# Optimization experiments

Hardware: AMD Instinct MI355X
Metric: run time of the kernel (lower is better)

The kernel has to match this reference:

```python
import jax, jax.numpy as jnp
import numpy as np

COND_EPS = 1e-12  # singularity threshold for the 2x2 Hessian determinant


def setup_inputs() -> dict:
    key = jax.random.key(0)
    k1, k2 = jax.random.split(key)
    b, h, w = 8, 1024, 1536
    # neur_beta_eme: non-negative-ish network output (forward clamps at 0 anyway)
    neur_beta_eme = jax.random.uniform(k1, (b, 1, h, w), dtype=jnp.float32) * 2.0
    base_detector_score = jax.random.normal(k2, (b, 1, h, w), dtype=jnp.float32)
    return {
        "neur_beta_eme": neur_beta_eme,
        "base_detector_score": base_detector_score,
        "n": 2048,
        "border_size": 16,
    }


def _gather(score_flat, y, x, w):
    # score_flat: [b, h*w]; y,x: [b,n] -> [b,n]
    return jnp.take_along_axis(score_flat, y * w + x, axis=-1)


def reference(neur_beta_eme, base_detector_score, n, border_size):
    b, _, h, w = base_detector_score.shape
    # NeSSDetector.forward: model(image)[-1].clamp(min=0)
    neur = jnp.maximum(neur_beta_eme, 0.0)
    score = base_detector_score

    # base_detector.get_extrema_mask: 3x3 NMS (local max) + border exclusion
    pooled = jax.lax.reduce_window(score, -jnp.inf, jax.lax.max,
                                   (1, 1, 3, 3), (1, 1, 1, 1), "SAME")
    ys = jnp.arange(h)
    xs = jnp.arange(w)
    border = (((ys >= border_size) & (ys < h - border_size))[:, None]
              & ((xs >= border_size) & (xs < w - border_size))[None, :])
    extrema_mask = (score == pooled) & border[None, None]

    # ness_extrema_map = exp(-neur_beta_eme) * extrema_mask
    ness = jnp.exp(-neur) * extrema_mask.astype(score.dtype)

    # topk over flattened spatial dims
    ness_flat = ness.reshape(b, -1)                      # [b, h*w]
    _, flat_cand_kp = jax.lax.top_k(ness_flat, n)        # [b, n]

    # flat2grid(flat, w) + 0.5  (pixel-center coords, (y, x) order)
    y = flat_cand_kp // w
    x = flat_cand_kp % w
    cand_kp = jnp.stack([y, x], axis=-1).astype(score.dtype) + 0.5  # [b, n, 2]

    # localize_keypoints_via_taylor: 3x3 finite-difference gradient/Hessian,
    # solve H @ inc = -g per keypoint (2x2 closed-form solve)
    sf = score.reshape(b, -1)
    yc = jnp.clip(y, 1, h - 2)
    xc = jnp.clip(x, 1, w - 2)
    s00 = _gather(sf, yc, xc, w)
    sp0 = _gather(sf, yc + 1, xc, w)
    sm0 = _gather(sf, yc - 1, xc, w)
    s0p = _gather(sf, yc, xc + 1, w)
    s0m = _gather(sf, yc, xc - 1, w)
    spp = _gather(sf, yc + 1, xc + 1, w)
    spm = _gather(sf, yc + 1, xc - 1, w)
    smp = _gather(sf, yc - 1, xc + 1, w)
    smm = _gather(sf, yc - 1, xc - 1, w)

    gy = 0.5 * (sp0 - sm0)
    gx = 0.5 * (s0p - s0m)
    hyy = sp0 - 2.0 * s00 + sm0
    hxx = s0p - 2.0 * s00 + s0m
    hxy = 0.25 * (spp - spm - smp + smm)

    det = hyy * hxx - hxy * hxy
    sing_mask = jnp.abs(det) > COND_EPS
    safe_det = jnp.where(sing_mask, det, 1.0)
    inc_y = -(hxx * gy - hxy * gx) / safe_det
    inc_x = -(hyy * gx - hxy * gy) / safe_det
    inc = jnp.stack([inc_y, inc_x], axis=-1)             # [b, n, 2]
    inc = jnp.clip(jnp.where(sing_mask[..., None], inc, 0.0), -0.5, 0.5)

    kp = cand_kp + inc                                   # [b, n, 2]

    # kp_neur_beta_eme = neur.view(b,-1).gather(-1, flat_cand_kp)
    kp_neur = jnp.take_along_axis(neur.reshape(b, -1), flat_cand_kp, axis=-1)

    return jnp.concatenate([kp, kp_neur[..., None]], axis=-1)  # [b, n, 3]
```

## Files before the change

### kernel.cpp

```cpp
#include <hip/hip_runtime.h>
#include <math.h>

typedef unsigned int u32;
typedef unsigned long long u64;

#define B 8
#define H 1024
#define W 1536
#define NPIX (H * W)
#define NK 2048
#define BORDER 16
#define NSEG 64
#define TY 8
#define NTILE 6
#define GRIDY 31
#define HBINS 512
#define TOPK_CAP 4096
#define SORT_N 4096
#define SORT_T 512
#define SEG_CAP_MAX 4096
#define CTR_PAD 32
#define IDX_MASK 0x1FFFFFu

#define OFF_TCOUNT 128
#define OFF_HIST   4096
#define OFF_SEGCNT 20480
#define OFF_KEYS   86016
#define OFF_SORTED 348160
#define OFF_CAND   479232

__global__ __launch_bounds__(256) void cand_k(const float* __restrict__ neur,
                                              const float* __restrict__ score,
                                              u32* __restrict__ candp,
                                              u32* __restrict__ segcnt,
                                              u32* __restrict__ hist, int seg_cap) {
    __shared__ u32 lh[HBINS];
    int tile = blockIdx.x;
    int b = blockIdx.z;
    int wave = threadIdx.x >> 6;
    int lane = threadIdx.x & 63;
    for (int i = threadIdx.x; i < HBINS; i += 256) lh[i] = 0;
    __syncthreads();

    int strip = blockIdx.y * 4 + wave;
    int y0 = BORDER + strip * TY;
    int x0 = tile * 256 + lane * 4;
    const float* s = score + (size_t)b * NPIX;
    const float* nb = neur + (size_t)b * NPIX;
    bool haveL = (tile > 0) && (lane == 0);
    bool haveR = (tile < NTILE - 1) && (lane == 63);

    float4 rv[TY + 2];
    float le[TY + 2], re[TY + 2];
    const float* base_row = s + (size_t)(y0 - 1) * W + x0;
    #pragma unroll
    for (int r = 0; r < TY + 2; ++r) rv[r] = *(const float4*)(base_row + (size_t)r * W);
    #pragma unroll
    for (int r = 0; r < TY + 2; ++r) {
        le[r] = haveL ? base_row[(size_t)r * W - 1] : 0.0f;
        re[r] = haveR ? base_row[(size_t)r * W + 4] : 0.0f;
    }

    bool xok[4];
    #pragma unroll
    for (int e = 0; e < 4; ++e) {
        int x = x0 + e;
        xok[e] = (x >= BORDER) && (x < W - BORDER);
    }

    u32 extbits = 0;
    {
        float4 hm, h0, hp;
        #pragma unroll
        for (int r = 0; r < 2; ++r) {
            float4 c = rv[r];
            float l = __shfl_up(c.w, 1); if (haveL) l = le[r];
            float rr = __shfl_down(c.x, 1); if (haveR) rr = re[r];
            float4 hh;
            hh.x = fmaxf(fmaxf(l, c.x), c.y);
            hh.y = fmaxf(fmaxf(c.x, c.y), c.z);
            hh.z = fmaxf(fmaxf(c.y, c.z), c.w);
            hh.w = fmaxf(fmaxf(c.z, c.w), rr);
            if (r == 0) hm = hh; else h0 = hh;
        }
        #pragma unroll
        for (int ys = 0; ys < TY; ++ys) {
            float4 c = rv[ys + 2];
            float l = __shfl_up(c.w, 1); if (haveL) l = le[ys + 2];
            float rr = __shfl_down(c.x, 1); if (haveR) rr = re[ys + 2];
            hp.x = fmaxf(fmaxf(l, c.x), c.y);
            hp.y = fmaxf(fmaxf(c.x, c.y), c.z);
            hp.z = fmaxf(fmaxf(c.y, c.z), c.w);
            hp.w = fmaxf(fmaxf(c.z, c.w), rr);
            float pv[4];
            pv[0] = fmaxf(fmaxf(hm.x, h0.x), hp.x);
            pv[1] = fmaxf(fmaxf(hm.y, h0.y), hp.y);
            pv[2] = fmaxf(fmaxf(hm.z, h0.z), hp.z);
            pv[3] = fmaxf(fmaxf(hm.w, h0.w), hp.w);
            float4 c0 = rv[ys + 1];
            float cv[4] = {c0.x, c0.y, c0.z, c0.w};
            #pragma unroll
            for (int e = 0; e < 4; ++e)
                if (xok[e] && cv[e] >= pv[e]) extbits |= (1u << (ys * 4 + e));
            hm = h0; h0 = hp;
        }
    }

    u32 c = (u32)__popc(extbits);
    u32 scan = c;
    #pragma unroll
    for (int off = 1; off < 64; off <<= 1) {
        u32 o = (u32)__shfl_up((int)scan, off, 64);
        if (lane >= off) scan += o;
    }
    u32 excl = scan - c;
    u32 tot = (u32)__shfl((int)scan, 63, 64);
    if (tot) {
        int seg = (strip * NTILE + tile) & (NSEG - 1);
        u32* ctr = &segcnt[(u32)(b * NSEG + seg) * CTR_PAD];
        u32 base = 0;
        if (lane == 63) base = atomicAdd(ctr, scan);
        base = (u32)__shfl((int)base, 63, 64);
        u32 pos0 = base + excl;
        u32 sbase = (u32)(b * NSEG + seg) * (u32)seg_cap;
        u32 idxbase = (u32)(y0 * W + x0);
        #pragma unroll
        for (int k = 0; k < 32; ++k) {
            if (extbits & (1u << k)) {
                u32 idx = idxbase + (u32)(k >> 2) * W + (u32)(k & 3);
                float nv = fmaxf(nb[idx], 0.0f);
                u32 fb = __float_as_uint(nv);
                u32 bin = fb >> 21; if (bin > HBINS - 1) bin = HBINS - 1;
                atomicAdd(&lh[bin], 1u);
                u32 p = pos0 + (u32)__popc(extbits & ((1u << k) - 1u));
                if ((int)p < seg_cap) candp[sbase + p] = (bin << 21) | idx;
            }
        }
    }
    __syncthreads();
    for (int i = threadIdx.x; i < HBINS; i += 256) {
        u32 v = lh[i];
        if (v) atomicAdd(&hist[(u32)b * HBINS + i], v);
    }
}

__global__ __launch_bounds__(256) void compact_k(const u32* __restrict__ candp,
                                                 const u32* __restrict__ segcnt,
                                                 const u32* __restrict__ hist,
                                                 const float* __restrict__ neur,
                                                 u64* __restrict__ keysout,
                                                 u32* tcount, int seg_cap) {
    __shared__ u32 piv_s;
    int seg = blockIdx.x;
    int b = blockIdx.y;
    int lane = threadIdx.x & 63;
    if (threadIdx.x < 64) {
        if (threadIdx.x == 0) piv_s = 0xFFFFFFFFu;
        u32 v[8];
        u32 s8 = 0;
        #pragma unroll
        for (int e = 0; e < 8; ++e) {
            v[e] = hist[(u32)b * HBINS + (u32)threadIdx.x * 8u + e];
            s8 += v[e];
        }
        u32 incl = s8;
        #pragma unroll
        for (int off = 1; off < 64; off <<= 1) {
            u32 o = (u32)__shfl_up((int)incl, off, 64);
            if (lane >= off) incl += o;
        }
        u32 excl = incl - s8;
        if (excl < NK && incl >= NK) {
            u32 cum = excl;
            u32 T = 0;
            #pragma unroll
            for (int e = 0; e < 8; ++e) {
                cum += v[e];
                if (cum >= NK) { T = (u32)threadIdx.x * 8u + e; break; }
            }
            piv_s = (T + 2u) << 21;
        }
    }
    __syncthreads();
    u32 piv = piv_s;
    const float* nb = neur + (size_t)b * NPIX;

    u32 cnt = segcnt[(u32)(b * NSEG + seg) * CTR_PAD];
    if ((int)cnt > seg_cap) cnt = (u32)seg_cap;
    u32 base = (u32)(b * NSEG + seg) * (u32)seg_cap;
    u32 iters = (cnt + 255u) / 256u;
    for (u32 it = 0; it < iters; ++it) {
        u32 i = it * 256u + threadIdx.x;
        bool f = false;
        u32 idx = 0;
        if (i < cnt) {
            u32 p = candp[base + i];
            f = (p < piv);
            idx = p & IDX_MASK;
        }
        u64 m = __ballot((int)f);
        if (m) {
            int leader = __ffsll((long long)m) - 1;
            u32 wbase = 0;
            if (lane == leader) wbase = atomicAdd(&tcount[b * CTR_PAD], (u32)__popcll(m));
            wbase = (u32)__shfl((int)wbase, leader, 64);
            if (f) {
                u32 pos = wbase + (u32)__popcll(m & ((1ull << (u32)lane) - 1ull));
                if (pos < TOPK_CAP) {
                    float nv = fmaxf(nb[idx], 0.0f);
                    float ness = (float)exp(-(double)nv);
                    keysout[(u32)b * TOPK_CAP + pos] =
                        ((u64)__float_as_uint(ness) << 32) | (u32)(~idx);
                }
            }
        }
    }
}

__device__ __forceinline__ u32 sw(u32 i) { return i + (i >> 4); }

__device__ __forceinline__ void cex(u64& a, u64& b, bool desc) {
    bool swp = desc ? (a < b) : (a > b);
    if (swp) { u64 tmp = a; a = b; b = tmp; }
}

__global__ __launch_bounds__(SORT_T) void sort_k(const u64* __restrict__ keysin,
                                                 const u32* __restrict__ tcount,
                                                 u64* __restrict__ sorted) {
    __shared__ u64 keys[SORT_N + (SORT_N >> 4)];
    int b = blockIdx.x;
    u32 t = threadIdx.x;
    u32 cnt = tcount[b * CTR_PAD];
    if (cnt > TOPK_CAP) cnt = TOPK_CAP;
    for (u32 i = t; i < SORT_N; i += SORT_T)
        keys[sw(i)] = (i < cnt) ? keysin[(u32)b * TOPK_CAP + i] : 0ull;
    __syncthreads();

    {
        u64 r[8];
        u32 base = t * 8u;
        #pragma unroll
        for (int e = 0; e < 8; ++e) r[e] = keys[sw(base + e)];
        cex(r[0], r[1], true);  cex(r[2], r[3], false);
        cex(r[4], r[5], true);  cex(r[6], r[7], false);
        cex(r[0], r[2], true);  cex(r[1], r[3], true);
        cex(r[4], r[6], false); cex(r[5], r[7], false);
        cex(r[0], r[1], true);  cex(r[2], r[3], true);
        cex(r[4], r[5], false); cex(r[6], r[7], false);
        bool d = ((base & 8u) == 0u);
        cex(r[0], r[4], d); cex(r[1], r[5], d); cex(r[2], r[6], d); cex(r[3], r[7], d);
        cex(r[0], r[2], d); cex(r[1], r[3], d); cex(r[4], r[6], d); cex(r[5], r[7], d);
        cex(r[0], r[1], d); cex(r[2], r[3], d); cex(r[4], r[5], d); cex(r[6], r[7], d);
        #pragma unroll
        for (int e = 0; e < 8; ++e) keys[sw(base + e)] = r[e];
    }
    __syncthreads();

    for (u32 k = 16; k <= SORT_N; k <<= 1) {
        u32 j = k >> 1;
        while (j >= 4) {
            u32 j0 = j >> 2;
            u32 base = ((t & ~(j0 - 1u)) << 3) | (t & (j0 - 1u));
            bool d = ((base & k) == 0u);
            u64 r[8];
            #pragma unroll
            for (int e = 0; e < 8; ++e) r[e] = keys[sw(base + (u32)e * j0)];
            cex(r[0], r[4], d); cex(r[1], r[5], d); cex(r[2], r[6], d); cex(r[3], r[7], d);
            cex(r[0], r[2], d); cex(r[1], r[3], d); cex(r[4], r[6], d); cex(r[5], r[7], d);
            cex(r[0], r[1], d); cex(r[2], r[3], d); cex(r[4], r[5], d); cex(r[6], r[7], d);
            #pragma unroll
            for (int e = 0; e < 8; ++e) keys[sw(base + (u32)e * j0)] = r[e];
            __syncthreads();
            j >>= 3;
        }
        if (j == 2) {
            #pragma unroll
            for (u32 m = 0; m < 2; ++m) {
                u32 vt = t + m * SORT_T;
                u32 base = vt << 2;
                bool d = ((base & k) == 0u);
                u64 r0 = keys[sw(base)], r1 = keys[sw(base + 1)];
                u64 r2 = keys[sw(base + 2)], r3 = keys[sw(base + 3)];
                cex(r0, r2, d); cex(r1, r3, d);
                cex(r0, r1, d); cex(r2, r3, d);
                keys[sw(base)] = r0; keys[sw(base + 1)] = r1;
                keys[sw(base + 2)] = r2; keys[sw(base + 3)] = r3;
            }
            __syncthreads();
        } else if (j == 1) {
            #pragma unroll
            for (u32 m = 0; m < 4; ++m) {
                u32 vt = t + m * SORT_T;
                u32 base = vt << 1;
                bool d = ((base & k) == 0u);
                u64 r0 = keys[sw(base)], r1 = keys[sw(base + 1)];
                cex(r0, r1, d);
                keys[sw(base)] = r0; keys[sw(base + 1)] = r1;
            }
            __syncthreads();
        }
    }

    for (u32 i = t; i < NK; i += SORT_T)
        sorted[(u32)b * NK + i] = keys[sw(i)];
}

__global__ __launch_bounds__(256) void refine_k(const float* __restrict__ neur,
                                                const float* __restrict__ score,
                                                const u64* __restrict__ sorted,
                                                float* __restrict__ out) {
    int b = blockIdx.y;
    u32 i = blockIdx.x * 256u + threadIdx.x;
    const float* s = score + (size_t)b * NPIX;
    const float* nb = neur + (size_t)b * NPIX;
    u64 key = sorted[(u32)b * NK + i];
    u32 idx = ~(u32)key;
    int y = (int)(idx / W), x = (int)(idx % W);
    int yc = min(max(y, 1), H - 2), xc = min(max(x, 1), W - 2);
    int p = yc * W + xc;
    float s00 = s[p], sp0 = s[p + W], sm0 = s[p - W], s0p = s[p + 1], s0m = s[p - 1];
    float spp = s[p + W + 1], spm = s[p + W - 1], smp = s[p - W + 1], smm = s[p - W - 1];
    float gy = 0.5f * (sp0 - sm0);
    float gx = 0.5f * (s0p - s0m);
    float hyy = sp0 - 2.0f * s00 + sm0;
    float hxx = s0p - 2.0f * s00 + s0m;
    float hxy = 0.25f * (spp - spm - smp + smm);
    float det = hyy * hxx - hxy * hxy;
    bool sing = fabsf(det) > 1e-12f;
    float sd = sing ? det : 1.0f;
    float iy = -(hxx * gy - hxy * gx) / sd;
    float ix = -(hyy * gx - hxy * gy) / sd;
    if (!sing) { iy = 0.0f; ix = 0.0f; }
    iy = fminf(fmaxf(iy, -0.5f), 0.5f);
    ix = fminf(fmaxf(ix, -0.5f), 0.5f);
    size_t o = ((size_t)b * NK + (size_t)i) * 3;
    out[o] = (float)y + 0.5f + iy;
    out[o + 1] = (float)x + 0.5f + ix;
    out[o + 2] = fmaxf(nb[idx], 0.0f);
}

extern "C" void kernel_launch(void* const* d_in, const int* in_sizes, int n_in,
                              void* d_out, int out_size, void* d_ws, size_t ws_size,
                              hipStream_t stream) {
    const float* neur = (const float*)d_in[0];
    const float* score = (const float*)d_in[1];
    float* out = (float*)d_out;
    char* ws = (char*)d_ws;
    u32* tcount = (u32*)(ws + OFF_TCOUNT);
    u32* hist = (u32*)(ws + OFF_HIST);
    u32* segcnt = (u32*)(ws + OFF_SEGCNT);
    u64* keysbuf = (u64*)(ws + OFF_KEYS);
    u64* sorted = (u64*)(ws + OFF_SORTED);
    u32* candp = (u32*)(ws + OFF_CAND);

    size_t avail = ws_size > OFF_CAND ? ws_size - OFF_CAND : 0;
    long long cap_ll = (long long)(avail / (4ull * B * NSEG));
    int seg_cap = cap_ll > SEG_CAP_MAX ? SEG_CAP_MAX : (int)cap_ll;

    hipMemsetAsync(ws, 0, OFF_KEYS, stream);
    cand_k<<<dim3(NTILE, GRIDY, B), 256, 0, stream>>>(neur, score, candp, segcnt, hist, seg_cap);
    compact_k<<<dim3(NSEG, B), 256, 0, stream>>>(candp, segcnt, hist, neur, keysbuf, tcount, seg_cap);
    sort_k<<<B, SORT_T, 0, stream>>>(keysbuf, tcount, sorted);
    refine_k<<<dim3(NK / 256, B), 256, 0, stream>>>(neur, score, sorted, out);
}
```

Before: 189.1 us.

## Replace per-batch bitonic sort with parallel rank-counting and scatter by rank

Removes the single-block-per-batch bitonic sort, whose many barrier-separated passes occupy only eight workgroups. In its place a rank kernel runs many 1024-thread blocks: each key counts how many keys in a tile are larger and accumulates that count atomically. Refine then writes each candidate whose rank is below the top-k count directly to its output slot. The candidate kernel also preloads neur rows as float4 vectors instead of doing scattered scalar loads. The cost is O(N^2) comparisons and a larger memset that now clears the key buffer so empty slots hold zero keys.

```diff
diff --git a/kernel.cpp b/kernel.cpp
--- a/kernel.cpp
+++ b/kernel.cpp
@@ -16,8 +16,6 @@
 #define GRIDY 31
 #define HBINS 512
 #define TOPK_CAP 4096
-#define SORT_N 4096
-#define SORT_T 512
 #define SEG_CAP_MAX 4096
 #define CTR_PAD 32
 #define IDX_MASK 0x1FFFFFu
@@ -25,8 +23,8 @@
 #define OFF_TCOUNT 128
 #define OFF_HIST   4096
 #define OFF_SEGCNT 20480
-#define OFF_KEYS   86016
-#define OFF_SORTED 348160
+#define OFF_RANK   86016
+#define OFF_KEYS   217088
 #define OFF_CAND   479232
 
 __global__ __launch_bounds__(256) void cand_k(const float* __restrict__ neur,
@@ -51,10 +49,14 @@
     bool haveR = (tile < NTILE - 1) && (lane == 63);
 
     float4 rv[TY + 2];
+    float4 nvv[TY];
     float le[TY + 2], re[TY + 2];
     const float* base_row = s + (size_t)(y0 - 1) * W + x0;
+    const float* nrow = nb + (size_t)y0 * W + x0;
     #pragma unroll
     for (int r = 0; r < TY + 2; ++r) rv[r] = *(const float4*)(base_row + (size_t)r * W);
+    #pragma unroll
+    for (int r = 0; r < TY; ++r) nvv[r] = *(const float4*)(nrow + (size_t)r * W);
     #pragma unroll
     for (int r = 0; r < TY + 2; ++r) {
         le[r] = haveL ? base_row[(size_t)r * W - 1] : 0.0f;
@@ -127,11 +129,14 @@
         #pragma unroll
         for (int k = 0; k < 32; ++k) {
             if (extbits & (1u << k)) {
-                u32 idx = idxbase + (u32)(k >> 2) * W + (u32)(k & 3);
-                float nv = fmaxf(nb[idx], 0.0f);
+                const int ro = k >> 2, e = k & 3;
+                float4 nq = nvv[ro];
+                float raw = (e == 0) ? nq.x : (e == 1) ? nq.y : (e == 2) ? nq.z : nq.w;
+                float nv = fmaxf(raw, 0.0f);
                 u32 fb = __float_as_uint(nv);
                 u32 bin = fb >> 21; if (bin > HBINS - 1) bin = HBINS - 1;
                 atomicAdd(&lh[bin], 1u);
+                u32 idx = idxbase + (u32)ro * W + (u32)e;
                 u32 p = pos0 + (u32)__popc(extbits & ((1u << k) - 1u));
                 if ((int)p < seg_cap) candp[sbase + p] = (bin << 21) | idx;
             }
@@ -217,104 +222,34 @@
     }
 }
 
-__device__ __forceinline__ u32 sw(u32 i) { return i + (i >> 4); }
-
-__device__ __forceinline__ void cex(u64& a, u64& b, bool desc) {
-    bool swp = desc ? (a < b) : (a > b);
-    if (swp) { u64 tmp = a; a = b; b = tmp; }
-}
-
-__global__ __launch_bounds__(SORT_T) void sort_k(const u64* __restrict__ keysin,
-                                                 const u32* __restrict__ tcount,
-                                                 u64* __restrict__ sorted) {
-    __shared__ u64 keys[SORT_N + (SORT_N >> 4)];
-    int b = blockIdx.x;
-    u32 t = threadIdx.x;
-    u32 cnt = tcount[b * CTR_PAD];
-    if (cnt > TOPK_CAP) cnt = TOPK_CAP;
-    for (u32 i = t; i < SORT_N; i += SORT_T)
-        keys[sw(i)] = (i < cnt) ? keysin[(u32)b * TOPK_CAP + i] : 0ull;
+__global__ __launch_bounds__(1024) void rank_k(const u64* __restrict__ keys,
+                                               u32* __restrict__ rank) {
+    __shared__ u64 jk[1024];
+    int b = blockIdx.z;
+    u32 i = blockIdx.x * 1024u + threadIdx.x;
+    u64 ki = keys[(u32)b * TOPK_CAP + i];
+    jk[threadIdx.x] = keys[(u32)b * TOPK_CAP + blockIdx.y * 1024u + threadIdx.x];
     __syncthreads();
-
-    {
-        u64 r[8];
-        u32 base = t * 8u;
-        #pragma unroll
-        for (int e = 0; e < 8; ++e) r[e] = keys[sw(base + e)];
-        cex(r[0], r[1], true);  cex(r[2], r[3], false);
-        cex(r[4], r[5], true);  cex(r[6], r[7], false);
-        cex(r[0], r[2], true);  cex(r[1], r[3], true);
-        cex(r[4], r[6], false); cex(r[5], r[7], false);
-        cex(r[0], r[1], true);  cex(r[2], r[3], true);
-        cex(r[4], r[5], false); cex(r[6], r[7], false);
-        bool d = ((base & 8u) == 0u);
-        cex(r[0], r[4], d); cex(r[1], r[5], d); cex(r[2], r[6], d); cex(r[3], r[7], d);
-        cex(r[0], r[2], d); cex(r[1], r[3], d); cex(r[4], r[6], d); cex(r[5], r[7], d);
-        cex(r[0], r[1], d); cex(r[2], r[3], d); cex(r[4], r[5], d); cex(r[6], r[7], d);
-        #pragma unroll
-        for (int e = 0; e < 8; ++e) keys[sw(base + e)] = r[e];
-    }
-    __syncthreads();
-
-    for (u32 k = 16; k <= SORT_N; k <<= 1) {
-        u32 j = k >> 1;
-        while (j >= 4) {
-            u32 j0 = j >> 2;
-            u32 base = ((t & ~(j0 - 1u)) << 3) | (t & (j0 - 1u));
-            bool d = ((base & k) == 0u);
-            u64 r[8];
-            #pragma unroll
-            for (int e = 0; e < 8; ++e) r[e] = keys[sw(base + (u32)e * j0)];
-            cex(r[0], r[4], d); cex(r[1], r[5], d); cex(r[2], r[6], d); cex(r[3], r[7], d);
-            cex(r[0], r[2], d); cex(r[1], r[3], d); cex(r[4], r[6], d); cex(r[5], r[7], d);
-            cex(r[0], r[1], d); cex(r[2], r[3], d); cex(r[4], r[5], d); cex(r[6], r[7], d);
-            #pragma unroll
-            for (int e = 0; e < 8; ++e) keys[sw(base + (u32)e * j0)] = r[e];
-            __syncthreads();
-            j >>= 3;
-        }
-        if (j == 2) {
-            #pragma unroll
-            for (u32 m = 0; m < 2; ++m) {
-                u32 vt = t + m * SORT_T;
-                u32 base = vt << 2;
-                bool d = ((base & k) == 0u);
-                u64 r0 = keys[sw(base)], r1 = keys[sw(base + 1)];
-                u64 r2 = keys[sw(base + 2)], r3 = keys[sw(base + 3)];
-                cex(r0, r2, d); cex(r1, r3, d);
-                cex(r0, r1, d); cex(r2, r3, d);
-                keys[sw(base)] = r0; keys[sw(base + 1)] = r1;
-                keys[sw(base + 2)] = r2; keys[sw(base + 3)] = r3;
-            }
-            __syncthreads();
-        } else if (j == 1) {
-            #pragma unroll
-            for (u32 m = 0; m < 4; ++m) {
-                u32 vt = t + m * SORT_T;
-                u32 base = vt << 1;
-                bool d = ((base & k) == 0u);
-                u64 r0 = keys[sw(base)], r1 = keys[sw(base + 1)];
-                cex(r0, r1, d);
-                keys[sw(base)] = r0; keys[sw(base + 1)] = r1;
-            }
-            __syncthreads();
-        }
-    }
-
-    for (u32 i = t; i < NK; i += SORT_T)
-        sorted[(u32)b * NK + i] = keys[sw(i)];
+    u32 r = 0;
+    #pragma unroll 8
+    for (int j = 0; j < 1024; ++j) r += (jk[j] > ki) ? 1u : 0u;
+    if (r) atomicAdd(&rank[(u32)b * TOPK_CAP + i], r);
 }
 
 __global__ __launch_bounds__(256) void refine_k(const float* __restrict__ neur,
                                                 const float* __restrict__ score,
-                                                const u64* __restrict__ sorted,
+                                                const u64* __restrict__ keys,
+                                                const u32* __restrict__ rank,
                                                 float* __restrict__ out) {
     int b = blockIdx.y;
     u32 i = blockIdx.x * 256u + threadIdx.x;
+    u32 r = rank[(u32)b * TOPK_CAP + i];
+    if (r >= NK) return;
     const float* s = score + (size_t)b * NPIX;
     const float* nb = neur + (size_t)b * NPIX;
-    u64 key = sorted[(u32)b * NK + i];
+    u64 key = keys[(u32)b * TOPK_CAP + i];
     u32 idx = ~(u32)key;
+    if (idx >= (u32)NPIX) return;
     int y = (int)(idx / W), x = (int)(idx % W);
     int yc = min(max(y, 1), H - 2), xc = min(max(x, 1), W - 2);
     int p = yc * W + xc;
@@ -333,7 +268,7 @@
     if (!sing) { iy = 0.0f; ix = 0.0f; }
     iy = fminf(fmaxf(iy, -0.5f), 0.5f);
     ix = fminf(fmaxf(ix, -0.5f), 0.5f);
-    size_t o = ((size_t)b * NK + (size_t)i) * 3;
+    size_t o = ((size_t)b * NK + (size_t)r) * 3;
     out[o] = (float)y + 0.5f + iy;
     out[o + 1] = (float)x + 0.5f + ix;
     out[o + 2] = fmaxf(nb[idx], 0.0f);
@@ -349,17 +284,17 @@
     u32* tcount = (u32*)(ws + OFF_TCOUNT);
     u32* hist = (u32*)(ws + OFF_HIST);
     u32* segcnt = (u32*)(ws + OFF_SEGCNT);
+    u32* rank = (u32*)(ws + OFF_RANK);
     u64* keysbuf = (u64*)(ws + OFF_KEYS);
-    u64* sorted = (u64*)(ws + OFF_SORTED);
     u32* candp = (u32*)(ws + OFF_CAND);
 
     size_t avail = ws_size > OFF_CAND ? ws_size - OFF_CAND : 0;
     long long cap_ll = (long long)(avail / (4ull * B * NSEG));
     int seg_cap = cap_ll > SEG_CAP_MAX ? SEG_CAP_MAX : (int)cap_ll;
 
-    hipMemsetAsync(ws, 0, OFF_KEYS, stream);
+    hipMemsetAsync(ws, 0, OFF_CAND, stream);
     cand_k<<<dim3(NTILE, GRIDY, B), 256, 0, stream>>>(neur, score, candp, segcnt, hist, seg_cap);
     compact_k<<<dim3(NSEG, B), 256, 0, stream>>>(candp, segcnt, hist, neur, keysbuf, tcount, seg_cap);
-    sort_k<<<B, SORT_T, 0, stream>>>(keysbuf, tcount, sorted);
-    refine_k<<<dim3(NK / 256, B), 256, 0, stream>>>(neur, score, sorted, out);
-}
+    rank_k<<<dim3(TOPK_CAP / 1024, TOPK_CAP / 1024, B), 1024, 0, stream>>>(keysbuf, rank);
+    refine_k<<<dim3(TOPK_CAP / 256, B), 256, 0, stream>>>(neur, score, keysbuf, rank, out);
+}
```

After: 178.1 us. -5.8%, faster.
